# Kernel tuning notes

Hardware: AMD Instinct MI355X
Metric: run time of the kernel (lower is better)

Reference implementation:

```python
import jax, jax.numpy as jnp
import numpy as np

VOCAB = 50257
DIM = 1024


def setup_inputs() -> dict:
    key = jax.random.key(0)
    k1, k2, k3, k4 = jax.random.split(key, 4)
    # Padded filter bank: row i holds filter i (true length VOCAB-DIM+i+1);
    # only element 0 of each filter ever contributes (one-hot input at index 0).
    filters = jax.random.uniform(k1, (DIM, VOCAB), dtype=jnp.float32)
    w_t = jax.random.uniform(k2, (DIM, DIM), dtype=jnp.float32)
    w_h = jax.random.uniform(k3, (DIM, DIM), dtype=jnp.float32)
    inp = jax.random.randint(k4, (1,), 0, VOCAB)  # unused by the module's forward
    return {"input": inp, "filters": filters, "w_t": w_t, "w_h": w_h}


def reference(input, filters, w_t, w_h):
    dim = filters.shape[0]
    f0 = filters[:, 0]
    # conv1d(one_hot(0), filter_i) = [filter_i[0], 0, ..., 0] with output
    # length dim - i; so max = max(f0, 0) except the last filter (length-1
    # output) where max = f0 exactly.
    is_last = jnp.arange(dim) == dim - 1
    y_k = jnp.where(is_last, f0, jnp.maximum(f0, 0.0))
    t = jax.nn.sigmoid(y_k @ w_t.T)  # F.linear(y_k, w_t)
    g = jax.nn.relu(y_k @ w_h.T)     # F.linear(y_k, w_h)
    z = t * g + (1.0 - t) * y_k
    return jax.nn.log_softmax(z, axis=0)
```

## Files before the change

kernel.cpp:

```cpp
#include <hip/hip_runtime.h>
#include <math.h>

#define DIM   1024
#define VOCAB 50257

__global__ __launch_bounds__(256) void compute_z_kernel(
    const float* __restrict__ filters,
    const float* __restrict__ w_t,
    const float* __restrict__ w_h,
    float* __restrict__ z)
{
    __shared__ float yk[DIM];
    const int tid = threadIdx.x;

    for (int d = tid; d < DIM; d += 256) {
        float f = filters[(size_t)d * VOCAB];
        yk[d] = (d == DIM - 1) ? f : fmaxf(f, 0.0f);
    }
    __syncthreads();

    const int wave = tid >> 6;
    const int lane = tid & 63;
    const int row  = blockIdx.x * 4 + wave;

    const float* __restrict__ wt = w_t + (size_t)row * DIM;
    const float* __restrict__ wh = w_h + (size_t)row * DIM;

    float acc_t = 0.0f, acc_h = 0.0f;
    #pragma unroll
    for (int k = 0; k < DIM; k += 256) {
        const int idx = k + lane * 4;
        float4 a = *(const float4*)(wt + idx);
        float4 b = *(const float4*)(wh + idx);
        float4 y = *(const float4*)(&yk[idx]);
        acc_t += a.x * y.x + a.y * y.y + a.z * y.z + a.w * y.w;
        acc_h += b.x * y.x + b.y * y.y + b.z * y.z + b.w * y.w;
    }

    #pragma unroll
    for (int off = 32; off > 0; off >>= 1) {
        acc_t += __shfl_down(acc_t, off);
        acc_h += __shfl_down(acc_h, off);
    }

    if (lane == 0) {
        float t = 1.0f / (1.0f + expf(-acc_t));
        float g = fmaxf(acc_h, 0.0f);
        z[row] = t * g + (1.0f - t) * yk[row];
    }
}

__global__ __launch_bounds__(1024) void log_softmax_kernel(
    const float* __restrict__ z,
    float* __restrict__ out)
{
    __shared__ float red_max[16];
    __shared__ float red_sum[16];
    const int tid  = threadIdx.x;
    const int wave = tid >> 6;
    const int lane = tid & 63;

    float v = z[tid];

    float m = v;
    #pragma unroll
    for (int off = 32; off > 0; off >>= 1)
        m = fmaxf(m, __shfl_down(m, off));
    if (lane == 0) red_max[wave] = m;
    __syncthreads();
    if (wave == 0) {
        float mm = (lane < 16) ? red_max[lane] : -INFINITY;
        #pragma unroll
        for (int off = 8; off > 0; off >>= 1)
            mm = fmaxf(mm, __shfl_down(mm, off));
        if (lane == 0) red_max[0] = mm;
    }
    __syncthreads();
    const float gmax = red_max[0];

    float e = expf(v - gmax);
    float s = e;
    #pragma unroll
    for (int off = 32; off > 0; off >>= 1)
        s += __shfl_down(s, off);
    if (lane == 0) red_sum[wave] = s;
    __syncthreads();
    if (wave == 0) {
        float ss = (lane < 16) ? red_sum[lane] : 0.0f;
        #pragma unroll
        for (int off = 8; off > 0; off >>= 1)
            ss += __shfl_down(ss, off);
        if (lane == 0) red_sum[0] = ss;
    }
    __syncthreads();

    out[tid] = v - gmax - logf(red_sum[0]);
}

extern "C" void kernel_launch(void* const* d_in, const int* in_sizes, int n_in,
                              void* d_out, int out_size, void* d_ws, size_t ws_size,
                              hipStream_t stream) {
    const float* filters = (const float*)d_in[1];
    const float* w_t     = (const float*)d_in[2];
    const float* w_h     = (const float*)d_in[3];
    float* out = (float*)d_out;
    float* z   = (float*)d_ws;

    compute_z_kernel<<<256, 256, 0, stream>>>(filters, w_t, w_h, z);
    log_softmax_kernel<<<1, 1024, 0, stream>>>(z, out);
}
```

Baseline: 242.6 us.

## Fuse log-softmax into matvec kernel via last-block atomic counter

Merges the separate log-softmax kernel into the gated matvec kernel. Each block increments a global counter after writing its z entries, and the last block to finish computes the log-softmax over all 1024 values with 256 threads handling four elements each. This removes a kernel launch and the gap between the two kernels. In exchange it adds a memset of the counter, thread fences and an atomic per block.

```diff
diff --git a/kernel.cpp b/kernel.cpp
--- a/kernel.cpp
+++ b/kernel.cpp
@@ -4,13 +4,17 @@
 #define DIM   1024
 #define VOCAB 50257
 
-__global__ __launch_bounds__(256) void compute_z_kernel(
+__global__ __launch_bounds__(256) void fused_embed_kernel(
     const float* __restrict__ filters,
     const float* __restrict__ w_t,
     const float* __restrict__ w_h,
-    float* __restrict__ z)
+    float* __restrict__ z,
+    unsigned int* __restrict__ counter,
+    float* __restrict__ out)
 {
     __shared__ float yk[DIM];
+    __shared__ float red[4];
+    __shared__ int   last_flag;
     const int tid = threadIdx.x;
 
     for (int d = tid; d < DIM; d += 256) {
@@ -26,75 +30,71 @@
     const float* __restrict__ wt = w_t + (size_t)row * DIM;
     const float* __restrict__ wh = w_h + (size_t)row * DIM;
 
-    float acc_t = 0.0f, acc_h = 0.0f;
+    float at = 0.0f, ah = 0.0f;
     #pragma unroll
     for (int k = 0; k < DIM; k += 256) {
         const int idx = k + lane * 4;
         float4 a = *(const float4*)(wt + idx);
         float4 b = *(const float4*)(wh + idx);
         float4 y = *(const float4*)(&yk[idx]);
-        acc_t += a.x * y.x + a.y * y.y + a.z * y.z + a.w * y.w;
-        acc_h += b.x * y.x + b.y * y.y + b.z * y.z + b.w * y.w;
+        at += a.x * y.x + a.y * y.y + a.z * y.z + a.w * y.w;
+        ah += b.x * y.x + b.y * y.y + b.z * y.z + b.w * y.w;
+    }
+    #pragma unroll
+    for (int off = 32; off > 0; off >>= 1) {
+        at += __shfl_down(at, off);
+        ah += __shfl_down(ah, off);
+    }
+    if (lane == 0) {
+        float t = 1.0f / (1.0f + expf(-at));
+        float g = fmaxf(ah, 0.0f);
+        z[row] = t * g + (1.0f - t) * yk[row];
     }
 
+    __threadfence();
+    __syncthreads();
+    if (tid == 0) {
+        unsigned int old = atomicAdd(counter, 1u);
+        __threadfence();
+        last_flag = (old == 255u);
+    }
+    __syncthreads();
+    if (!last_flag) return;
+
+    float v[4];
     #pragma unroll
-    for (int off = 32; off > 0; off >>= 1) {
-        acc_t += __shfl_down(acc_t, off);
-        acc_h += __shfl_down(acc_h, off);
-    }
+    for (int j = 0; j < 4; j++) v[j] = z[tid + j * 256];
 
-    if (lane == 0) {
-        float t = 1.0f / (1.0f + expf(-acc_t));
-        float g = fmaxf(acc_h, 0.0f);
-        z[row] = t * g + (1.0f - t) * yk[row];
-    }
-}
-
-__global__ __launch_bounds__(1024) void log_softmax_kernel(
-    const float* __restrict__ z,
-    float* __restrict__ out)
-{
-    __shared__ float red_max[16];
-    __shared__ float red_sum[16];
-    const int tid  = threadIdx.x;
-    const int wave = tid >> 6;
-    const int lane = tid & 63;
-
-    float v = z[tid];
-
-    float m = v;
+    float m = fmaxf(fmaxf(v[0], v[1]), fmaxf(v[2], v[3]));
     #pragma unroll
     for (int off = 32; off > 0; off >>= 1)
         m = fmaxf(m, __shfl_down(m, off));
-    if (lane == 0) red_max[wave] = m;
+    if (lane == 0) red[wave] = m;
     __syncthreads();
-    if (wave == 0) {
-        float mm = (lane < 16) ? red_max[lane] : -INFINITY;
-        #pragma unroll
-        for (int off = 8; off > 0; off >>= 1)
-            mm = fmaxf(mm, __shfl_down(mm, off));
-        if (lane == 0) red_max[0] = mm;
+    if (tid == 0) {
+        red[0] = fmaxf(fmaxf(red[0], red[1]), fmaxf(red[2], red[3]));
     }
     __syncthreads();
-    const float gmax = red_max[0];
+    const float gmax = red[0];
+    __syncthreads();
 
-    float e = expf(v - gmax);
-    float s = e;
+    float s = 0.0f;
+    #pragma unroll
+    for (int j = 0; j < 4; j++) s += expf(v[j] - gmax);
     #pragma unroll
     for (int off = 32; off > 0; off >>= 1)
         s += __shfl_down(s, off);
-    if (lane == 0) red_sum[wave] = s;
+    if (lane == 0) red[wave] = s;
     __syncthreads();
-    if (wave == 0) {
-        float ss = (lane < 16) ? red_sum[lane] : 0.0f;
-        #pragma unroll
-        for (int off = 8; off > 0; off >>= 1)
-            ss += __shfl_down(ss, off);
-        if (lane == 0) red_sum[0] = ss;
+    if (tid == 0) {
+        red[0] = red[0] + red[1] + red[2] + red[3];
     }
     __syncthreads();
+    const float lse = logf(red[0]);
 
-    out[tid] = v - gmax - logf(red_sum[0]);
+    #pragma unroll
+    for (int j = 0; j < 4; j++)
+        out[tid + j * 256] = v[j] - gmax - lse;
 }
 
 extern "C" void kernel_launch(void* const* d_in, const int* in_sizes, int n_in,
@@ -105,7 +105,8 @@
     const float* w_h     = (const float*)d_in[3];
     float* out = (float*)d_out;
     float* z   = (float*)d_ws;
+    unsigned int* counter = (unsigned int*)((char*)d_ws + 4096);
 
-    compute_z_kernel<<<256, 256, 0, stream>>>(filters, w_t, w_h, z);
-    log_softmax_kernel<<<1, 1024, 0, stream>>>(z, out);
+    hipMemsetAsync(counter, 0, sizeof(unsigned int), stream);
+    fused_embed_kernel<<<256, 256, 0, stream>>>(filters, w_t, w_h, z, counter, out);
 }
```

Result: slower. 261.3 us (+7.7%).
